# Kernel tuning notes

Hardware: AMD Instinct MI355X
Metric: run time of the kernel (lower is better)

The kernel has to match this reference:

```python
import jax, jax.numpy as jnp
import numpy as np

V, NSEG, MAXLEN, D, H = 32000, 2, 512, 768, 12
HS = D // H  # head_size = 64
B, T, NMASK = 16, 512, 20
LN_EPS = 1e-5


def setup_inputs() -> dict:
    key = jax.random.key(0)
    ks = jax.random.split(key, 16)
    s = 0.02
    return {
        "sequence": jax.random.randint(ks[0], (B, T), 0, V),
        "segment": jax.random.randint(ks[1], (B, T), 0, NSEG),
        "attn_mask": jax.random.randint(ks[2], (B, T), 0, 2).astype(jnp.int32),
        "masked_pos": jax.random.randint(ks[3], (B, NMASK), 0, T),
        "tok_emb": jax.random.normal(ks[4], (V, D), jnp.float32) * s,
        "seg_emb": jax.random.normal(ks[5], (NSEG, D), jnp.float32) * s,
        "pos_emb": jax.random.normal(ks[6], (MAXLEN, D), jnp.float32) * s,
        "ln_g": jnp.ones((D,), jnp.float32),
        "ln_b": jnp.zeros((D,), jnp.float32),
        "Wq": jax.random.normal(ks[7], (H, D, HS), jnp.float32) * s,
        "Wk": jax.random.normal(ks[8], (H, D, HS), jnp.float32) * s,
        "Wv": jax.random.normal(ks[9], (H, D, HS), jnp.float32) * s,
        "W_lm": jax.random.normal(ks[10], (D, V), jnp.float32) * s,
        "b_lm": jnp.zeros((V,), jnp.float32),
        "W_cls": jax.random.normal(ks[11], (D, 2), jnp.float32) * s,
        "b_cls": jnp.zeros((2,), jnp.float32),
    }


def reference(sequence, segment, attn_mask, masked_pos,
              tok_emb, seg_emb, pos_emb, ln_g, ln_b,
              Wq, Wk, Wv, W_lm, b_lm, W_cls, b_cls):
    Tlen = sequence.shape[1]
    # --- BERTEmbedding (dropout = identity in eval) ---
    emb = tok_emb[sequence] + seg_emb[segment] + pos_emb[jnp.arange(Tlen)][None]  # [B,T,D]
    mu = jnp.mean(emb, axis=-1, keepdims=True)
    var = jnp.mean(jnp.square(emb - mu), axis=-1, keepdims=True)
    x = (emb - mu) * jax.lax.rsqrt(var + LN_EPS) * ln_g + ln_b  # [B,T,D]

    # --- Multi-head attention (heads batched instead of Python loop) ---
    q = jnp.einsum('btd,hds->bhts', x, Wq)
    k = jnp.einsum('btd,hds->bhts', x, Wk)
    v = jnp.einsum('btd,hds->bhts', x, Wv)
    wei = jnp.einsum('bhts,bhus->bhtu', q, k) * (HS ** -0.5)  # [B,H,T,T]
    # original: wei.masked_fill(attn_mask[:, :, None] == 0, -1e-11) -> masks over query dim
    wei = jnp.where(attn_mask[:, None, :, None] == 0, jnp.float32(-1e-11), wei)
    wei = jax.nn.softmax(wei, axis=-1)
    out = jnp.einsum('bhtu,bhus->bhts', wei, v)  # [B,H,T,HS]
    x = out.transpose(0, 2, 1, 3).reshape(out.shape[0], Tlen, H * HS)  # cat heads -> [B,T,D]

    # --- Output heads ---
    x_masked = jnp.take_along_axis(x, masked_pos[:, :, None], axis=1)  # [B,NMASK,D]
    logits_lm = x_masked @ W_lm + b_lm          # [B,NMASK,V]
    logits_clsf = x[:, 0, :] @ W_cls + b_cls    # [B,2]
    return (logits_lm, logits_clsf)
```

## Files before the change

### kernel.cpp

```cpp
#include <hip/hip_runtime.h>
#include <hip/hip_bf16.h>

#define V_     32000
#define NSEG_  2
#define MAXLEN_ 512
#define D_     768
#define H_     12
#define HS_    64
#define B_     16
#define T_     512
#define NMASK_ 20
#define LN_EPS_ 1e-5f

typedef __hip_bfloat16 bf16;
typedef unsigned short ushortT;
typedef __attribute__((ext_vector_type(8))) short short8;
typedef __attribute__((ext_vector_type(4))) float f32x4;
typedef __attribute__((ext_vector_type(4))) unsigned int u32x4;
typedef __attribute__((ext_vector_type(4))) unsigned short u16x4;

__device__ __forceinline__ ushortT f2bu(float f) {
    bf16 h = __float2bfloat16(f);
    return *reinterpret_cast<ushortT*>(&h);
}

__global__ void k_embed_ln(const int* __restrict__ seq, const int* __restrict__ seg,
                           const float* __restrict__ tok, const float* __restrict__ sege,
                           const float* __restrict__ pos, const float* __restrict__ g,
                           const float* __restrict__ bb, ushortT* __restrict__ xb) {
    int row = blockIdx.x;
    int t = row & (T_ - 1);
    int tid = threadIdx.x;
    __shared__ float wsum[3], wsq[3];

    int sidx = seq[row];
    int gidx = seg[row];

    f32x4 e = *(const f32x4*)(tok  + (size_t)sidx * D_ + tid * 4);
    f32x4 e2 = *(const f32x4*)(sege + (size_t)gidx * D_ + tid * 4);
    f32x4 e3 = *(const f32x4*)(pos  + (size_t)t    * D_ + tid * 4);
    e = e + e2 + e3;

    float ls = e.x + e.y + e.z + e.w;
    float lq = e.x * e.x + e.y * e.y + e.z * e.z + e.w * e.w;
    #pragma unroll
    for (int o = 32; o > 0; o >>= 1) {
        ls += __shfl_down(ls, o);
        lq += __shfl_down(lq, o);
    }
    if ((tid & 63) == 0) { wsum[tid >> 6] = ls; wsq[tid >> 6] = lq; }
    __syncthreads();
    float s  = wsum[0] + wsum[1] + wsum[2];
    float sq = wsq[0] + wsq[1] + wsq[2];
    float mean = s * (1.0f / D_);
    float var  = sq * (1.0f / D_) - mean * mean;
    float rstd = rsqrtf(var + LN_EPS_);

    f32x4 g4 = *(const f32x4*)(g  + tid * 4);
    f32x4 b4 = *(const f32x4*)(bb + tid * 4);
    f32x4 x4;
    x4.x = (e.x - mean) * rstd * g4.x + b4.x;
    x4.y = (e.y - mean) * rstd * g4.y + b4.y;
    x4.z = (e.z - mean) * rstd * g4.z + b4.z;
    x4.w = (e.w - mean) * rstd * g4.w + b4.w;
    u16x4 ov = {f2bu(x4.x), f2bu(x4.y), f2bu(x4.z), f2bu(x4.w)};
    *(u16x4*)(xb + (size_t)row * D_ + tid * 4) = ov;
}

__global__ void k_prep_wqkv(const float* __restrict__ Wq, const float* __restrict__ Wk,
                            const float* __restrict__ Wv, ushortT* __restrict__ Wt) {
    int blk = blockIdx.x;
    int which = blk / H_, h = blk % H_;
    int kc = blockIdx.y * 64;
    const float* W = (which == 0) ? Wq : (which == 1) ? Wk : Wv;
    __shared__ float tile[64][65];
    int tid = threadIdx.x, c = tid & 63, rgrp = tid >> 6;
    for (int kk = rgrp; kk < 64; kk += 4)
        tile[kk][c] = W[((size_t)h * D_ + kc + kk) * HS_ + c];
    __syncthreads();
    for (int ss = rgrp; ss < 64; ss += 4)
        Wt[((size_t)which * D_ + h * HS_ + ss) * D_ + kc + c] = f2bu(tile[c][ss]);
}

__global__ void k_gather_xm(const float* __restrict__ x2, const int* __restrict__ masked_pos,
                            ushortT* __restrict__ xm) {
    int r = blockIdx.x;
    int tid = threadIdx.x;
    if (r < B_ * NMASK_) {
        int b = r / NMASK_, m = r % NMASK_;
        int t = masked_pos[b * NMASK_ + m];
        for (int d = tid; d < D_; d += 256)
            xm[(size_t)r * D_ + d] = f2bu(x2[((size_t)b * T_ + t) * D_ + d]);
    } else {
        for (int d = tid; d < D_; d += 256)
            xm[(size_t)r * D_ + d] = 0;
    }
}

__device__ __forceinline__ void stage_chunk(const ushortT* __restrict__ src, int row_stride,
                                            int r0, int k0, ushortT* dst, int w, int lane) {
    #pragma unroll
    for (int i = 0; i < 2; ++i) {
        int slot = w * 64 + lane + i * 256;
        int row = slot >> 2;
        int cs = ((slot & 3) ^ (row & 3)) * 8;
        __builtin_amdgcn_global_load_lds(
            (const __attribute__((address_space(1))) void*)(src + (size_t)(r0 + row) * row_stride + k0 + cs),
            (__attribute__((address_space(3))) void*)(dst + (w * 64 + i * 256) * 8),
            16, 0, 0);
    }
}

__device__ __forceinline__ void gemm128_2ph(const ushortT* __restrict__ A,
                                            const ushortT* __restrict__ Bt,
                                            int m0, int n0,
                                            ushortT* lds,
                                            f32x4 acc[4][4]) {
    const int NT = D_ / 32;
    int tid = threadIdx.x;
    int lane = tid & 63, w = tid >> 6;
    int wr = (w >> 1) * 64, wc = (w & 1) * 64;
    int l16 = lane & 15, lk = lane >> 4;
    int sw = (lk ^ (l16 & 3)) * 8;

    #pragma unroll
    for (int i = 0; i < 4; ++i)
        #pragma unroll
        for (int j = 0; j < 4; ++j)
            acc[i][j] = (f32x4){0.f, 0.f, 0.f, 0.f};

    stage_chunk(A, D_, m0, 0, lds, w, lane);
    stage_chunk(Bt, D_, n0, 0, lds + 4096, w, lane);
    asm volatile("s_waitcnt vmcnt(0)" ::: "memory");
    __builtin_amdgcn_s_barrier();

    for (int t = 0; t < NT; ++t) {
        int cur = (t & 1) * 8192;
        int nxt = 8192 - cur;
        if (t + 1 < NT) {
            stage_chunk(A, D_, m0, (t + 1) * 32, lds + nxt, w, lane);
            stage_chunk(Bt, D_, n0, (t + 1) * 32, lds + nxt + 4096, w, lane);
        }

        const ushortT* Asc = lds + cur;
        const ushortT* Bsc = lds + cur + 4096;
        short8 a[4], bfr[4];
        #pragma unroll
        for (int i = 0; i < 4; ++i) {
            a[i]   = *(const short8*)(Asc + (wr + i * 16 + l16) * 32 + sw);
            bfr[i] = *(const short8*)(Bsc + (wc + i * 16 + l16) * 32 + sw);
        }
        #pragma unroll
        for (int i = 0; i < 4; ++i)
            #pragma unroll
            for (int j = 0; j < 4; ++j)
                acc[i][j] = __builtin_amdgcn_mfma_f32_16x16x32_bf16(a[i], bfr[j], acc[i][j], 0, 0, 0);

        asm volatile("s_waitcnt vmcnt(0)" ::: "memory");
        __builtin_amdgcn_s_barrier();
    }
}

__global__ __launch_bounds__(256, 4)
void k_gemm_qkv(const ushortT* __restrict__ xb, const ushortT* __restrict__ WcatT,
                ushortT* __restrict__ qb, ushortT* __restrict__ kb,
                ushortT* __restrict__ vb) {
    __shared__ ushortT lds[128 * 136];
    f32x4 acc[4][4];
    int lin = (blockIdx.x & 7) * 144 + (blockIdx.x >> 3);
    int n0 = (lin % 18) * 128, m0 = (lin / 18) * 128;
    gemm128_2ph(xb, WcatT, m0, n0, lds, acc);

    int tid = threadIdx.x;
    int lane = tid & 63, w = tid >> 6;
    int wr = (w >> 1) * 64, wc = (w & 1) * 64;
    int l16 = lane & 15, lk = lane >> 4;

    #pragma unroll
    for (int j = 0; j < 4; ++j) {
        int n = wc + j * 16 + l16;
        #pragma unroll
        for (int i = 0; i < 4; ++i) {
            #pragma unroll
            for (int r = 0; r < 4; ++r) {
                int m = wr + i * 16 + lk * 4 + r;
                lds[m * 136 + n] = f2bu(acc[i][j][r]);
            }
        }
    }
    __syncthreads();

    int which = n0 / D_;
    int nrem0 = n0 - which * D_;
    ushortT* outp = (which == 0) ? qb : (which == 1) ? kb : vb;
    int b = m0 >> 9;
    int t0 = m0 & (T_ - 1);
    #pragma unroll
    for (int p = 0; p < 8; ++p) {
        int chunk = p * 256 + tid;
        int row = chunk >> 4;
        int nc = (chunk & 15) * 8;
        int h = (nrem0 >> 6) + (nc >> 6);
        int s0 = nc & 63;
        u32x4 v = *(const u32x4*)(&lds[row * 136 + nc]);
        *(u32x4*)(outp + ((size_t)(b * H_ + h) * T_ + (t0 + row)) * HS_ + s0) = v;
    }
}

__global__ __launch_bounds__(256, 4)
void k_gemm_lm(const ushortT* __restrict__ xm, const float* __restrict__ Wlm,
               const float* __restrict__ blm, float* __restrict__ out) {
    const int NT = D_ / 32;
    __shared__ ushortT As[2][4096];
    __shared__ ushortT Bs[2][128 * 36];
    f32x4 acc[4][4];

    int bid = blockIdx.x;
    const int q = 93, r = 6;
    int xcd = bid & 7, idx = bid >> 3;
    int lin = (xcd < r) ? xcd * (q + 1) + idx : r * (q + 1) + (xcd - r) * q + idx;
    int nt = lin / 3, mt = lin - nt * 3;
    int m0 = mt * 128, n0 = nt * 128;

    int tid = threadIdx.x;
    int lane = tid & 63, w = tid >> 6;
    int wr = (w >> 1) * 64, wc = (w & 1) * 64;
    int l16 = lane & 15, lk = lane >> 4;
    int sw = (lk ^ (l16 & 3)) * 8;
    int n_l = tid & 127;
    int kkg = tid >> 7;

    #pragma unroll
    for (int i = 0; i < 4; ++i)
        #pragma unroll
        for (int j = 0; j < 4; ++j)
            acc[i][j] = (f32x4){0.f, 0.f, 0.f, 0.f};

    stage_chunk(xm, D_, m0, 0, As[0], w, lane);
    {
        #pragma unroll
        for (int g = 0; g < 4; ++g) {
            int kk0 = (g * 2 + kkg) * 4;
            const float* Wp = Wlm + (size_t)kk0 * V_ + n0 + n_l;
            u16x4 pk = {f2bu(Wp[0]), f2bu(Wp[(size_t)V_]), f2bu(Wp[(size_t)2 * V_]), f2bu(Wp[(size_t)3 * V_])};
            *(u16x4*)(&Bs[0][n_l * 36 + kk0]) = pk;
        }
    }
    asm volatile("s_waitcnt vmcnt(0) lgkmcnt(0)" ::: "memory");
    __builtin_amdgcn_s_barrier();

    for (int t = 0; t < NT; ++t) {
        int cur = t & 1, nx = cur ^ 1;
        float bf[16];
        if (t + 1 < NT) {
            stage_chunk(xm, D_, m0, (t + 1) * 32, As[nx], w, lane);
            int k0 = (t + 1) * 32;
            #pragma unroll
            for (int g = 0; g < 4; ++g) {
                int kk0 = (g * 2 + kkg) * 4;
                const float* Wp = Wlm + (size_t)(k0 + kk0) * V_ + n0 + n_l;
                bf[g * 4 + 0] = Wp[0];
                bf[g * 4 + 1] = Wp[(size_t)V_];
                bf[g * 4 + 2] = Wp[(size_t)2 * V_];
                bf[g * 4 + 3] = Wp[(size_t)3 * V_];
            }
        }

        short8 a[4], bfr[4];
        #pragma unroll
        for (int i = 0; i < 4; ++i) {
            a[i]   = *(const short8*)(&As[cur][(wr + i * 16 + l16) * 32 + sw]);
            bfr[i] = *(const short8*)(&Bs[cur][(wc + i * 16 + l16) * 36 + lk * 8]);
        }
        #pragma unroll
        for (int i = 0; i < 4; ++i)
            #pragma unroll
            for (int j = 0; j < 4; ++j)
                acc[i][j] = __builtin_amdgcn_mfma_f32_16x16x32_bf16(a[i], bfr[j], acc[i][j], 0, 0, 0);

        if (t + 1 < NT) {
            #pragma unroll
            for (int g = 0; g < 4; ++g) {
                int kk0 = (g * 2 + kkg) * 4;
                u16x4 pk = {f2bu(bf[g * 4]), f2bu(bf[g * 4 + 1]), f2bu(bf[g * 4 + 2]), f2bu(bf[g * 4 + 3])};
                *(u16x4*)(&Bs[nx][n_l * 36 + kk0]) = pk;
            }
        }
        asm volatile("s_waitcnt vmcnt(0) lgkmcnt(0)" ::: "memory");
        __builtin_amdgcn_s_barrier();
    }

    #pragma unroll
    for (int j = 0; j < 4; ++j) {
        int n = n0 + wc + j * 16 + l16;
        float bias = blm[n];
        #pragma unroll
        for (int i = 0; i < 4; ++i) {
            #pragma unroll
            for (int r2 = 0; r2 < 4; ++r2) {
                int m = m0 + wr + i * 16 + lk * 4 + r2;
                if (m < B_ * NMASK_)
                    out[(size_t)m * V_ + n] = acc[i][j][r2] + bias;
            }
        }
    }
}

__global__ __launch_bounds__(256, 4)
void k_attn_mfma(const ushortT* __restrict__ qb, const ushortT* __restrict__ kb,
                 const ushortT* __restrict__ vb, const int* __restrict__ attn_mask,
                 float* __restrict__ x2) {
    int lin = (blockIdx.x & 7) * 192 + (blockIdx.x >> 3);
    int qt = lin & 7, bh = lin >> 3;
    int b = bh / H_, h = bh % H_;
    int tid = threadIdx.x, lane = tid & 63, w = tid >> 6;
    int l16 = lane & 15, lk = lane >> 4;

    __shared__ ushortT QP[64][72];
    __shared__ ushortT Ks[64][72];
    __shared__ ushortT Vts[64][72];
    __shared__ float mskS[64];

    const ushortT* Qg = qb + ((size_t)bh * T_ + qt * 64) * HS_;
    #pragma unroll
    for (int i = 0; i < 2; ++i) {
        int slot = tid + i * 256;
        int r = slot >> 3, c8 = (slot & 7) * 8;
        *(u32x4*)(&QP[r][c8]) = *(const u32x4*)(Qg + (size_t)r * HS_ + c8);
    }
    if (tid < 64)
        mskS[tid] = attn_mask[b * T_ + qt * 64 + tid] ? 0.125f : 0.0f;
    __syncthreads();

    short8 aq[2];
    #pragma unroll
    for (int ks = 0; ks < 2; ++ks)
        aq[ks] = *(const short8*)(&QP[w * 16 + l16][ks * 32 + lk * 8]);
    float mrow[4];
    #pragma unroll
    for (int r = 0; r < 4; ++r)
        mrow[r] = mskS[w * 16 + lk * 4 + r];

    float lsum[4];
    f32x4 accO[4];
    #pragma unroll
    for (int r = 0; r < 4; ++r) lsum[r] = 0.f;
    #pragma unroll
    for (int j = 0; j < 4; ++j)
        accO[j] = (f32x4){0.f, 0.f, 0.f, 0.f};

    for (int kt = 0; kt < 8; ++kt) {
        __syncthreads();
        {
            int r = tid >> 2, c = (tid & 3) * 16;
            const ushortT* Kg = kb + ((size_t)bh * T_ + kt * 64 + r) * HS_ + c;
            *(u32x4*)(&Ks[r][c])     = *(const u32x4*)(Kg);
            *(u32x4*)(&Ks[r][c + 8]) = *(const u32x4*)(Kg + 8);
        }
        {
            int r = lane;
            int c = w * 16;
            const ushortT* Vg = vb + ((size_t)bh * T_ + kt * 64 + r) * HS_ + c;
            short8 v0 = *(const short8*)(Vg);
            short8 v1 = *(const short8*)(Vg + 8);
            #pragma unroll
            for (int e = 0; e < 8; ++e) Vts[c + e][r]     = (ushortT)v0[e];
            #pragma unroll
            for (int e = 0; e < 8; ++e) Vts[c + 8 + e][r] = (ushortT)v1[e];
        }
        __syncthreads();

        f32x4 accS[4];
        #pragma unroll
        for (int j = 0; j < 4; ++j)
            accS[j] = (f32x4){0.f, 0.f, 0.f, 0.f};
        #pragma unroll
        for (int ks = 0; ks < 2; ++ks) {
            short8 bk[4];
            #pragma unroll
            for (int j = 0; j < 4; ++j)
                bk[j] = *(const short8*)(&Ks[j * 16 + l16][ks * 32 + lk * 8]);
            #pragma unroll
            for (int j = 0; j < 4; ++j)
                accS[j] = __builtin_amdgcn_mfma_f32_16x16x32_bf16(aq[ks], bk[j], accS[j], 0, 0, 0);
        }

        #pragma unroll
        for (int r = 0; r < 4; ++r) {
            int rowl = lk * 4 + r;
            float m = mrow[r];
            float p0 = __expf(accS[0][r] * m);
            float p1 = __expf(accS[1][r] * m);
            float p2 = __expf(accS[2][r] * m);
            float p3 = __expf(accS[3][r] * m);
            lsum[r] += (p0 + p1) + (p2 + p3);
            QP[w * 16 + rowl][0 * 16 + l16] = f2bu(p0);
            QP[w * 16 + rowl][1 * 16 + l16] = f2bu(p1);
            QP[w * 16 + rowl][2 * 16 + l16] = f2bu(p2);
            QP[w * 16 + rowl][3 * 16 + l16] = f2bu(p3);
        }

        #pragma unroll
        for (int ks2 = 0; ks2 < 2; ++ks2) {
            short8 ap = *(const short8*)(&QP[w * 16 + l16][ks2 * 32 + lk * 8]);
            short8 bv[4];
            #pragma unroll
            for (int j = 0; j < 4; ++j)
                bv[j] = *(const short8*)(&Vts[j * 16 + l16][ks2 * 32 + lk * 8]);
            #pragma unroll
            for (int j = 0; j < 4; ++j)
                accO[j] = __builtin_amdgcn_mfma_f32_16x16x32_bf16(ap, bv[j], accO[j], 0, 0, 0);
        }
    }

    #pragma unroll
    for (int r = 0; r < 4; ++r) {
        float s = lsum[r];
        #pragma unroll
        for (int off = 1; off < 16; off <<= 1)
            s += __shfl_xor(s, off);
        float inv = 1.0f / s;
        int t = qt * 64 + w * 16 + lk * 4 + r;
        float* outp = x2 + ((size_t)b * T_ + t) * D_ + h * HS_;
        #pragma unroll
        for (int j = 0; j < 4; ++j)
            outp[j * 16 + l16] = accO[j][r] * inv;
    }
}

__global__ void k_cls(const float* __restrict__ x2, const float* __restrict__ Wc,
                      const float* __restrict__ bc, float* __restrict__ out) {
    int b = blockIdx.x;
    int tid = threadIdx.x;
    __shared__ float red0[4], red1[4];
    float a0 = 0.f, a1 = 0.f;
    const float* xr = x2 + (size_t)b * T_ * D_;
    for (int d = tid; d < D_; d += 256) {
        float x = xr[d];
        a0 += x * Wc[d * 2];
        a1 += x * Wc[d * 2 + 1];
    }
    #pragma unroll
    for (int o = 32; o > 0; o >>= 1) {
        a0 += __shfl_down(a0, o);
        a1 += __shfl_down(a1, o);
    }
    if ((tid & 63) == 0) { red0[tid >> 6] = a0; red1[tid >> 6] = a1; }
    __syncthreads();
    if (tid == 0)
        out[b * 2]     = red0[0] + red0[1] + red0[2] + red0[3] + bc[0];
    if (tid == 1)
        out[b * 2 + 1] = red1[0] + red1[1] + red1[2] + red1[3] + bc[1];
}

extern "C" void kernel_launch(void* const* d_in, const int* in_sizes, int n_in,
                              void* d_out, int out_size, void* d_ws, size_t ws_size,
                              hipStream_t stream) {
    const int* seq        = (const int*)d_in[0];
    const int* seg        = (const int*)d_in[1];
    const int* attn_mask  = (const int*)d_in[2];
    const int* masked_pos = (const int*)d_in[3];
    const float* tok  = (const float*)d_in[4];
    const float* sege = (const float*)d_in[5];
    const float* pos  = (const float*)d_in[6];
    const float* ln_g = (const float*)d_in[7];
    const float* ln_b = (const float*)d_in[8];
    const float* Wq   = (const float*)d_in[9];
    const float* Wk   = (const float*)d_in[10];
    const float* Wv   = (const float*)d_in[11];
    const float* Wlm  = (const float*)d_in[12];
    const float* blm  = (const float*)d_in[13];
    const float* Wc   = (const float*)d_in[14];
    const float* bc   = (const float*)d_in[15];

    float* out_lm  = (float*)d_out;
    float* out_cls = out_lm + (size_t)B_ * NMASK_ * V_;

    const size_t XSZ = (size_t)B_ * T_ * D_;
    float* ws = (float*)d_ws;
    float*   x2   = ws;
    ushortT* base = (ushortT*)(ws + XSZ);
    ushortT* xb    = base;
    ushortT* qb    = base + XSZ;
    ushortT* kb    = base + 2 * XSZ;
    ushortT* vb    = base + 3 * XSZ;
    ushortT* WcatT = base + 4 * XSZ;
    ushortT* xm    = base;

    k_embed_ln<<<B_ * T_, 192, 0, stream>>>(seq, seg, tok, sege, pos, ln_g, ln_b, xb);
    k_prep_wqkv<<<dim3(3 * H_, 12), 256, 0, stream>>>(Wq, Wk, Wv, WcatT);
    k_gemm_qkv<<<1152, 256, 0, stream>>>(xb, WcatT, qb, kb, vb);
    k_attn_mfma<<<192 * 8, 256, 0, stream>>>(qb, kb, vb, attn_mask, x2);
    k_gather_xm<<<384, 256, 0, stream>>>(x2, masked_pos, xm);
    k_gemm_lm<<<750, 256, 0, stream>>>(xm, Wlm, blm, out_lm);
    k_cls<<<B_, 256, 0, stream>>>(x2, Wc, bc, out_cls);
}
```

Baseline: 149.1 us.

## Deepen LM-head GEMM prefetch to two stages with triple-buffered A tiles

The LM-head GEMM now prefetches A tiles and fp32 W_lm values two K-steps ahead. A uses a triple LDS buffer and W uses two register buffers. The in-loop full vmcnt(0) wait is dropped, so global loads can stay in flight across a barrier, with ordering left to in-order vmcnt and compiler-inserted waits. The extra registers and LDS come at a cost: launch bounds drop from 4 to 3 blocks per CU, lowering occupancy.

```diff
diff --git a/kernel.cpp b/kernel.cpp
--- a/kernel.cpp
+++ b/kernel.cpp
@@ -207,11 +207,11 @@
     }
 }
 
-__global__ __launch_bounds__(256, 4)
+__global__ __launch_bounds__(256, 3)
 void k_gemm_lm(const ushortT* __restrict__ xm, const float* __restrict__ Wlm,
                const float* __restrict__ blm, float* __restrict__ out) {
     const int NT = D_ / 32;
-    __shared__ ushortT As[2][4096];
+    __shared__ ushortT As3[3][4096];
     __shared__ ushortT Bs[2][128 * 36];
     f32x4 acc[4][4];
 
@@ -236,40 +236,47 @@
         for (int j = 0; j < 4; ++j)
             acc[i][j] = (f32x4){0.f, 0.f, 0.f, 0.f};
 
-    stage_chunk(xm, D_, m0, 0, As[0], w, lane);
-    {
-        #pragma unroll
-        for (int g = 0; g < 4; ++g) {
-            int kk0 = (g * 2 + kkg) * 4;
-            const float* Wp = Wlm + (size_t)kk0 * V_ + n0 + n_l;
-            u16x4 pk = {f2bu(Wp[0]), f2bu(Wp[(size_t)V_]), f2bu(Wp[(size_t)2 * V_]), f2bu(Wp[(size_t)3 * V_])};
-            *(u16x4*)(&Bs[0][n_l * 36 + kk0]) = pk;
-        }
-    }
-    asm volatile("s_waitcnt vmcnt(0) lgkmcnt(0)" ::: "memory");
+    const float* Wbase = Wlm + n0 + n_l;
+
+    float bw0[16], bw1[16];
+    stage_chunk(xm, D_, m0, 0, As3[0], w, lane);
+    #pragma unroll
+    for (int g = 0; g < 4; ++g) {
+        int kk0 = (g * 2 + kkg) * 4;
+        const float* Wp = Wbase + (size_t)kk0 * V_;
+        bw0[g * 4 + 0] = Wp[0];
+        bw0[g * 4 + 1] = Wp[(size_t)V_];
+        bw0[g * 4 + 2] = Wp[(size_t)2 * V_];
+        bw0[g * 4 + 3] = Wp[(size_t)3 * V_];
+    }
+    asm volatile("s_waitcnt vmcnt(0)" ::: "memory");
+    #pragma unroll
+    for (int g = 0; g < 4; ++g) {
+        int kk0 = (g * 2 + kkg) * 4;
+        u16x4 pk = {f2bu(bw0[g * 4]), f2bu(bw0[g * 4 + 1]), f2bu(bw0[g * 4 + 2]), f2bu(bw0[g * 4 + 3])};
+        *(u16x4*)(&Bs[0][n_l * 36 + kk0]) = pk;
+    }
+    stage_chunk(xm, D_, m0, 32, As3[1], w, lane);
+    #pragma unroll
+    for (int g = 0; g < 4; ++g) {
+        int kk0 = (g * 2 + kkg) * 4;
+        const float* Wp = Wbase + (size_t)(32 + kk0) * V_;
+        bw1[g * 4 + 0] = Wp[0];
+        bw1[g * 4 + 1] = Wp[(size_t)V_];
+        bw1[g * 4 + 2] = Wp[(size_t)2 * V_];
+        bw1[g * 4 + 3] = Wp[(size_t)3 * V_];
+    }
+    asm volatile("s_waitcnt lgkmcnt(0)" ::: "memory");
     __builtin_amdgcn_s_barrier();
 
     for (int t = 0; t < NT; ++t) {
         int cur = t & 1, nx = cur ^ 1;
-        float bf[16];
-        if (t + 1 < NT) {
-            stage_chunk(xm, D_, m0, (t + 1) * 32, As[nx], w, lane);
-            int k0 = (t + 1) * 32;
-            #pragma unroll
-            for (int g = 0; g < 4; ++g) {
-                int kk0 = (g * 2 + kkg) * 4;
-                const float* Wp = Wlm + (size_t)(k0 + kk0) * V_ + n0 + n_l;
-                bf[g * 4 + 0] = Wp[0];
-                bf[g * 4 + 1] = Wp[(size_t)V_];
-                bf[g * 4 + 2] = Wp[(size_t)2 * V_];
-                bf[g * 4 + 3] = Wp[(size_t)3 * V_];
-            }
-        }
+        const ushortT* Ac = As3[t % 3];
 
         short8 a[4], bfr[4];
         #pragma unroll
         for (int i = 0; i < 4; ++i) {
-            a[i]   = *(const short8*)(&As[cur][(wr + i * 16 + l16) * 32 + sw]);
+            a[i]   = *(const short8*)(Ac + (wr + i * 16 + l16) * 32 + sw);
             bfr[i] = *(const short8*)(&Bs[cur][(wc + i * 16 + l16) * 36 + lk * 8]);
         }
         #pragma unroll
@@ -278,15 +285,49 @@
             for (int j = 0; j < 4; ++j)
                 acc[i][j] = __builtin_amdgcn_mfma_f32_16x16x32_bf16(a[i], bfr[j], acc[i][j], 0, 0, 0);
 
+        if (t + 2 < NT) {
+            stage_chunk(xm, D_, m0, (t + 2) * 32, As3[(t + 2) % 3], w, lane);
+            int k0 = (t + 2) * 32;
+            if (cur == 0) {
+                #pragma unroll
+                for (int g = 0; g < 4; ++g) {
+                    int kk0 = (g * 2 + kkg) * 4;
+                    const float* Wp = Wbase + (size_t)(k0 + kk0) * V_;
+                    bw0[g * 4 + 0] = Wp[0];
+                    bw0[g * 4 + 1] = Wp[(size_t)V_];
+                    bw0[g * 4 + 2] = Wp[(size_t)2 * V_];
+                    bw0[g * 4 + 3] = Wp[(size_t)3 * V_];
+                }
+            } else {
+                #pragma unroll
+                for (int g = 0; g < 4; ++g) {
+                    int kk0 = (g * 2 + kkg) * 4;
+                    const float* Wp = Wbase + (size_t)(k0 + kk0) * V_;
+                    bw1[g * 4 + 0] = Wp[0];
+                    bw1[g * 4 + 1] = Wp[(size_t)V_];
+                    bw1[g * 4 + 2] = Wp[(size_t)2 * V_];
+                    bw1[g * 4 + 3] = Wp[(size_t)3 * V_];
+                }
+            }
+        }
         if (t + 1 < NT) {
-            #pragma unroll
-            for (int g = 0; g < 4; ++g) {
-                int kk0 = (g * 2 + kkg) * 4;
-                u16x4 pk = {f2bu(bf[g * 4]), f2bu(bf[g * 4 + 1]), f2bu(bf[g * 4 + 2]), f2bu(bf[g * 4 + 3])};
-                *(u16x4*)(&Bs[nx][n_l * 36 + kk0]) = pk;
+            if (nx == 0) {
+                #pragma unroll
+                for (int g = 0; g < 4; ++g) {
+                    int kk0 = (g * 2 + kkg) * 4;
+                    u16x4 pk = {f2bu(bw0[g * 4]), f2bu(bw0[g * 4 + 1]), f2bu(bw0[g * 4 + 2]), f2bu(bw0[g * 4 + 3])};
+                    *(u16x4*)(&Bs[0][n_l * 36 + kk0]) = pk;
+                }
+            } else {
+                #pragma unroll
+                for (int g = 0; g < 4; ++g) {
+                    int kk0 = (g * 2 + kkg) * 4;
+                    u16x4 pk = {f2bu(bw1[g * 4]), f2bu(bw1[g * 4 + 1]), f2bu(bw1[g * 4 + 2]), f2bu(bw1[g * 4 + 3])};
+                    *(u16x4*)(&Bs[1][n_l * 36 + kk0]) = pk;
+                }
             }
         }
-        asm volatile("s_waitcnt vmcnt(0) lgkmcnt(0)" ::: "memory");
+        asm volatile("s_waitcnt lgkmcnt(0)" ::: "memory");
         __builtin_amdgcn_s_barrier();
     }
 
```

New measurement: 147.0 us, median of 2. Within noise of the previous version (-1.4%).
